# Kernel optimization log

Hardware: AMD Instinct MI355X
Metric: run time of the kernel (lower is better)

## Reference

```python
import jax, jax.numpy as jnp
import numpy as np

GAMMA = 0.9
SCALE_BASE = 512.0


def _xpos(x, downscale=False):
    """XPOS rotary embedding (torchscale variant) applied to x: (B, L, D)."""
    B, L, D = x.shape
    half = D // 2
    # per-channel magnitude base: ((2i) + 0.4*D) / (1.4*D), i over even channels
    scale_vec = (jnp.arange(0, D, 2, dtype=jnp.float32) + 0.4 * D) / (1.4 * D)  # (half,)
    power = jnp.arange(L, dtype=jnp.float32) / SCALE_BASE                        # (L,)
    scale = scale_vec[None, :] ** power[:, None]                                 # (L, half)
    if downscale:
        scale = 1.0 / scale
    # fixed sinusoidal frequencies over `half` dims
    inv_freq = 1.0 / (10000.0 ** (jnp.arange(half, dtype=jnp.float32) / half))   # (half,)
    sinusoid = jnp.arange(L, dtype=jnp.float32)[:, None] * inv_freq[None, :]     # (L, half)
    sin = jnp.repeat(jnp.sin(sinusoid) * scale, 2, axis=-1)                      # (L, D) interleaved dup
    cos = jnp.repeat(jnp.cos(sinusoid) * scale, 2, axis=-1)
    # rotate_every_two: (x0,x1,x2,x3,...) -> (-x1,x0,-x3,x2,...)
    x_even = x[..., 0::2]
    x_odd = x[..., 1::2]
    rot = jnp.stack((-x_odd, x_even), axis=-1).reshape(x.shape)
    return x * cos + rot * sin


def _get_D(seq_len):
    n = jnp.arange(seq_len, dtype=jnp.float32)[:, None]
    m = jnp.arange(seq_len, dtype=jnp.float32)[None, :]
    D = GAMMA ** jnp.abs(n - m)  # non-causal decay, no NaNs since gamma > 0
    return D


def setup_inputs() -> dict:
    key = jax.random.key(0)
    k1, k2, k3, k4 = jax.random.split(key, 4)
    B, L, H, Dh = 8, 2048, 1024, 1024
    X = jax.random.normal(k1, (B, L, H), dtype=jnp.float32)
    W_Q = jax.random.normal(k2, (H, Dh), dtype=jnp.float32) / H
    W_K = jax.random.normal(k3, (H, Dh), dtype=jnp.float32) / H
    W_V = jax.random.normal(k4, (H, Dh), dtype=jnp.float32) / H
    return {"X": X, "W_Q": W_Q, "W_K": W_K, "W_V": W_V}


def reference(X, W_Q, W_K, W_V):
    B, L, H = X.shape
    D = _get_D(L)                       # (L, L)
    Q = _xpos(X @ W_Q)                  # (B, L, Dh)
    K = _xpos(X @ W_K, downscale=True)  # (B, L, Dh)
    V = X @ W_V                         # (B, L, Dv)
    scores = jnp.einsum('bqd,bkd->bqk', Q, K)   # (B, L, L)
    p_attn = jax.nn.softmax(scores, axis=-1)
    p_attn = p_attn * D[None, :, :]              # elementwise decay AFTER softmax
    return jnp.einsum('bqk,bkv->bqv', p_attn, V)
```

## Files before the change

### kernel.cpp

```cpp
#include <hip/hip_runtime.h>
#include <math.h>


#define LDIM 2048
#define HDIM 1024
#define MTOT 16384

typedef unsigned short u16;
typedef __attribute__((ext_vector_type(16))) float f32x16;
typedef __attribute__((ext_vector_type(8))) short s16x8;

#define GLD16(gp, lp) __builtin_amdgcn_global_load_lds( \
    (const __attribute__((address_space(1))) void*)(gp), \
    (__attribute__((address_space(3))) void*)(lp), 16, 0, 0)

__device__ __forceinline__ u16 f2bf(float f) {
    unsigned u = __float_as_uint(f);
    return (u16)((u + 0x7FFFu + ((u >> 16) & 1u)) >> 16);
}

__device__ __forceinline__ void sincos_rev(float ang, float* sn, float* cs) {
    double dr = (double)ang * 0.15915494309189535;
    dr -= __builtin_floor(dr);
    float fr = (float)dr;
    float s_, c_;
    asm("v_sin_f32 %0, %1" : "=v"(s_) : "v"(fr));
    asm("v_cos_f32 %0, %1" : "=v"(c_) : "v"(fr));
    *sn = s_; *cs = c_;
}

#define ROW32(reg, laneHi) (((reg) & 3) + 8 * ((reg) >> 2) + 4 * (laneHi))

__device__ __forceinline__ void gemm128(const u16* __restrict__ A, const u16* __restrict__ B,
                                        int lda, int ldb, int K, int m0, int n0,
                                        char* smem, int tid, f32x16 (*acc)[2])
{
    char* As = smem;
    char* Bs = smem + 128 * 128;
    const int wv = tid >> 6, ln = tid & 63;
    const int wm = wv >> 1, wn = wv & 1;
    const int lane31 = ln & 31, laneHi = ln >> 5;
    const int srow = wv * 8 + (ln >> 3);
    const int scol = ((ln & 7) ^ (ln >> 3)) * 8;

    const u16* ap[4];
    const u16* bp[4];
#pragma unroll
    for (int i = 0; i < 4; ++i) {
        ap[i] = A + (size_t)(m0 + i * 32 + srow) * lda + scol;
        bp[i] = B + (size_t)(n0 + i * 32 + srow) * ldb + scol;
    }

    int abyte[2], bbyte[2];
#pragma unroll
    for (int f = 0; f < 2; ++f) {
        const int row_a = wm * 64 + f * 32 + lane31;
        const int row_b = wn * 64 + f * 32 + lane31;
        const int slot = (laneHi ^ (lane31 & 7)) << 4;
        abyte[f] = row_a * 128 + slot;
        bbyte[f] = row_b * 128 + slot;
    }

    for (int k0 = 0; k0 < K; k0 += 64) {
        __syncthreads();
#pragma unroll
        for (int i = 0; i < 4; ++i) {
            GLD16(ap[i], As + (i * 32 + wv * 8) * 128);
            GLD16(bp[i], Bs + (i * 32 + wv * 8) * 128);
            ap[i] += 64; bp[i] += 64;
        }
        __syncthreads();
#pragma unroll
        for (int ks = 0; ks < 4; ++ks) {
            s16x8 af[2], bf[2];
#pragma unroll
            for (int f = 0; f < 2; ++f) {
                af[f] = *(const s16x8*)(As + (abyte[f] ^ (ks << 5)));
                bf[f] = *(const s16x8*)(Bs + (bbyte[f] ^ (ks << 5)));
            }
#pragma unroll
            for (int i = 0; i < 2; ++i)
#pragma unroll
                for (int j = 0; j < 2; ++j)
                    acc[i][j] = __builtin_amdgcn_mfma_f32_32x32x16_bf16(af[i], bf[j], acc[i][j], 0, 0, 0);
        }
    }
    __syncthreads();
}

__global__ __launch_bounds__(256) void cast_x(const float* __restrict__ X,
                                              u16* __restrict__ Xb, int n4)
{
    int i = blockIdx.x * 256 + threadIdx.x;
    const int stride = gridDim.x * 256;
    for (; i < n4; i += stride) {
        float4 v = ((const float4*)X)[i];
        ushort4 o = make_ushort4(f2bf(v.x), f2bf(v.y), f2bf(v.z), f2bf(v.w));
        ((ushort4*)Xb)[i] = o;
    }
}

__global__ __launch_bounds__(256) void transw(const float* __restrict__ Wq,
                                              const float* __restrict__ Wk,
                                              const float* __restrict__ Wv,
                                              u16* __restrict__ WT)
{
    __shared__ float L[64][65];
    const int z = blockIdx.z;
    const float* Wz = (z == 0) ? Wq : (z == 1) ? Wk : Wv;
    u16* Oz = WT + (size_t)z * HDIM * HDIM;
    const int k0 = blockIdx.y * 64, n0 = blockIdx.x * 64;
    const int t = threadIdx.x;
    const int r_ = t >> 4, c4 = (t & 15) * 4;
#pragma unroll
    for (int it = 0; it < 4; ++it) {
        const int row = it * 16 + r_;
        float4 v = *(const float4*)&Wz[(size_t)(k0 + row) * HDIM + n0 + c4];
        L[row][c4 + 0] = v.x; L[row][c4 + 1] = v.y;
        L[row][c4 + 2] = v.z; L[row][c4 + 3] = v.w;
    }
    __syncthreads();
#pragma unroll
    for (int it = 0; it < 4; ++it) {
        const int orow = it * 16 + r_;
        ushort4 o = make_ushort4(f2bf(L[c4 + 0][orow]), f2bf(L[c4 + 1][orow]),
                                 f2bf(L[c4 + 2][orow]), f2bf(L[c4 + 3][orow]));
        *(ushort4*)&Oz[(size_t)(n0 + orow) * HDIM + k0 + c4] = o;
    }
}

__global__ __launch_bounds__(256) void qkv_gemm(
    const u16* __restrict__ Xb, const u16* __restrict__ WT,
    u16* __restrict__ Qb, u16* __restrict__ Kb, u16* __restrict__ Vt)
{
    __shared__ __align__(16) char smem[128 * 136 * 2];
    const int bid = blockIdx.x;
    const int xcd = bid & 7, t = bid >> 3;
    const int m8 = t & 7;
    const int u_ = t >> 3;
    const int z  = u_ % 3;
    const int v_ = u_ / 3;
    const int n_ = v_ & 7;
    const int mh = v_ >> 3;
    const int m0 = (xcd * 16 + mh * 8 + m8) * 128;
    const int n0 = n_ * 128;
    const int tid = threadIdx.x;

    f32x16 acc[2][2] = {};

    gemm128(Xb, WT + (size_t)z * HDIM * HDIM, HDIM, HDIM, HDIM, m0, n0, smem, tid, acc);

    const int wv = tid >> 6, ln = tid & 63;
    const int wm = wv >> 1, wn = wv & 1;
    const int lane31 = ln & 31, laneHi = ln >> 5;
    u16* T = (u16*)smem;

    if (z < 2) {
        const float pwsgn = (z == 0) ? (1.f / 512.f) : (-1.f / 512.f);
#pragma unroll
        for (int fn = 0; fn < 2; ++fn) {
            const int gc = n0 + wn * 64 + fn * 32 + lane31;
            const int ih = gc >> 1;
            const float invf = exp2f(-13.287712379549449f * (1.f / 512.f) * (float)ih);
            const float l2sv = log2f(((float)(2 * ih) + 409.6f) * (1.f / 1433.6f));
            const float sgn = (gc & 1) ? 1.f : -1.f;
#pragma unroll
            for (int fm = 0; fm < 2; ++fm) {
#pragma unroll
                for (int reg = 0; reg < 16; ++reg) {
                    const int ml = wm * 64 + fm * 32 + ROW32(reg, laneHi);
                    const int lpos = (m0 + ml) & (LDIM - 1);
                    float c = acc[fm][fn][reg];
                    float p = __shfl_xor(c, 1);
                    float sn, cs;
                    sincos_rev((float)lpos * invf, &sn, &cs);
                    float scl = exp2f((float)lpos * pwsgn * l2sv);
                    T[ml * 136 + wn * 64 + fn * 32 + lane31] = f2bf((c * cs + sgn * p * sn) * scl);
                }
            }
        }
    } else {
#pragma unroll
        for (int fn = 0; fn < 2; ++fn)
#pragma unroll
            for (int fm = 0; fm < 2; ++fm)
#pragma unroll
                for (int reg = 0; reg < 16; ++reg)
                    T[(wn * 64 + fn * 32 + lane31) * 136 + wm * 64 + fm * 32 + ROW32(reg, laneHi)] =
                        f2bf(acc[fm][fn][reg]);
    }
    __syncthreads();

    const int row_ = tid >> 4, colb = (tid & 15) * 8;
    if (z < 2) {
        u16* Out = (z == 0) ? Qb : Kb;
#pragma unroll
        for (int g = 0; g < 8; ++g) {
            const int row = g * 16 + row_;
            s16x8 v = *(const s16x8*)&T[row * 136 + colb];
            *(s16x8*)&Out[(size_t)(m0 + row) * HDIM + n0 + colb] = v;
        }
    } else {
        const int b = m0 >> 11, l0 = m0 & (LDIM - 1);
#pragma unroll
        for (int g = 0; g < 8; ++g) {
            const int row = g * 16 + row_;
            s16x8 v = *(const s16x8*)&T[row * 136 + colb];
            *(s16x8*)&Vt[((size_t)b * HDIM + n0 + row) * LDIM + l0 + colb] = v;
        }
    }
}

__global__ __launch_bounds__(256) void qk_gemm(
    const u16* __restrict__ Q, const u16* __restrict__ Km,
    u16* __restrict__ Wm, float* __restrict__ Zp)
{
    __shared__ __align__(16) char smem[128 * 136 * 2];
    __shared__ float Zl[2][128];
    const int bid = blockIdx.x;
    const int b = bid & 7, t = bid >> 3;
    const int mt8 = t & 7;
    const int w_ = t >> 3;
    const int nt = w_ & 15;
    const int mtH = w_ >> 4;
    const int m0 = (mtH * 8 + mt8) * 128;
    const int n0 = nt * 128;
    const int tid = threadIdx.x;

    f32x16 acc[2][2] = {};

    gemm128(Q + (size_t)b * LDIM * HDIM, Km + (size_t)b * LDIM * HDIM,
            HDIM, HDIM, HDIM, m0, n0, smem, tid, acc);

    const int wv = tid >> 6, ln = tid & 63;
    const int wm = wv >> 1, wn = wv & 1;
    const int lane31 = ln & 31, laneHi = ln >> 5;
    u16* T = (u16*)smem;
    const float LOG2E = 1.4426950408889634f;
    const float LOG2G = -0.15200309344504997f;

    float psum[2][16];
#pragma unroll
    for (int fm = 0; fm < 2; ++fm)
#pragma unroll
        for (int reg = 0; reg < 16; ++reg) psum[fm][reg] = 0.f;

#pragma unroll
    for (int fm = 0; fm < 2; ++fm) {
#pragma unroll
        for (int fn = 0; fn < 2; ++fn) {
            const int gk = n0 + wn * 64 + fn * 32 + lane31;
#pragma unroll
            for (int reg = 0; reg < 16; ++reg) {
                const int mloc = wm * 64 + fm * 32 + ROW32(reg, laneHi);
                const int gq = m0 + mloc;
                float t1 = acc[fm][fn][reg] * LOG2E;
                float e = exp2f(t1);
                int dd = gq - gk; dd = dd < 0 ? -dd : dd;
                psum[fm][reg] += e;
                T[mloc * 136 + wn * 64 + fn * 32 + lane31] =
                    f2bf(exp2f(t1 + (float)dd * LOG2G));
            }
        }
    }
#pragma unroll
    for (int fm = 0; fm < 2; ++fm)
#pragma unroll
        for (int reg = 0; reg < 16; ++reg) {
            float s = psum[fm][reg];
            s += __shfl_xor(s, 1); s += __shfl_xor(s, 2);
            s += __shfl_xor(s, 4); s += __shfl_xor(s, 8);
            s += __shfl_xor(s, 16);
            if (lane31 == 0)
                Zl[wn][wm * 64 + fm * 32 + ROW32(reg, laneHi)] = s;
        }
    __syncthreads();

    const int row_ = tid >> 4, colb = (tid & 15) * 8;
#pragma unroll
    for (int g = 0; g < 8; ++g) {
        const int row = g * 16 + row_;
        s16x8 v = *(const s16x8*)&T[row * 136 + colb];
        *(s16x8*)&Wm[((size_t)b * LDIM + m0 + row) * LDIM + n0 + colb] = v;
    }
    if (tid < 128)
        Zp[((size_t)b * 16 + nt) * LDIM + m0 + tid] = Zl[0][tid] + Zl[1][tid];
}

__global__ __launch_bounds__(256) void pv_gemm(
    const u16* __restrict__ Wm, const u16* __restrict__ Vt,
    const float* __restrict__ Zp, float* __restrict__ Out)
{
    __shared__ __align__(16) char smem[128 * 136 * 2];
    __shared__ float Zinv[128];
    const int bid = blockIdx.x;
    const int b = bid & 7, t = bid >> 3;
    const int mt4 = t & 3;
    const int w_ = t >> 2;
    const int nt = w_ & 7;
    const int mtQ = w_ >> 3;
    const int m0 = (mtQ * 4 + mt4) * 128;
    const int n0 = nt * 128;
    const int tid = threadIdx.x;

    if (tid < 128) {
        float zz = 0.f;
#pragma unroll
        for (int nb = 0; nb < 16; ++nb)
            zz += Zp[((size_t)b * 16 + nb) * LDIM + m0 + tid];
        Zinv[tid] = 1.0f / zz;
    }

    f32x16 acc[2][2] = {};

    gemm128(Wm + (size_t)b * LDIM * LDIM, Vt + (size_t)b * HDIM * LDIM,
            LDIM, LDIM, LDIM, m0, n0, smem, tid, acc);

    const int wv = tid >> 6, ln = tid & 63;
    const int wm = wv >> 1, wn = wv & 1;
    const int lane31 = ln & 31, laneHi = ln >> 5;
    float* Ob = Out + (size_t)b * LDIM * HDIM;
#pragma unroll
    for (int fm = 0; fm < 2; ++fm)
#pragma unroll
        for (int fn = 0; fn < 2; ++fn) {
            const int gn = n0 + wn * 64 + fn * 32 + lane31;
#pragma unroll
            for (int reg = 0; reg < 16; ++reg) {
                const int row = wm * 64 + fm * 32 + ROW32(reg, laneHi);
                Ob[(size_t)(m0 + row) * HDIM + gn] = acc[fm][fn][reg] * Zinv[row];
            }
        }
}

extern "C" void kernel_launch(void* const* d_in, const int* in_sizes, int n_in,
                              void* d_out, int out_size, void* d_ws, size_t ws_size,
                              hipStream_t stream)
{
    (void)in_sizes; (void)n_in; (void)out_size; (void)ws_size;
    const float* X  = (const float*)d_in[0];
    const float* Wq = (const float*)d_in[1];
    const float* Wk = (const float*)d_in[2];
    const float* Wv = (const float*)d_in[3];
    char* ws = (char*)d_ws;
    const size_t MB = 1024 * 1024;

    u16* Wmat = (u16*)ws;
    u16* Xb   = (u16*)ws;
    u16* WT   = (u16*)(ws + 32 * MB);
    u16* Qb   = (u16*)(ws + 64 * MB);
    u16* Kb   = (u16*)(ws + 96 * MB);
    u16* Vt   = (u16*)(ws + 128 * MB);
    float* Zp = (float*)(ws + 160 * MB);

    cast_x<<<2048, 256, 0, stream>>>(X, Xb, MTOT * HDIM / 4);
    transw<<<dim3(16, 16, 3), 256, 0, stream>>>(Wq, Wk, Wv, WT);
    qkv_gemm<<<3072, 256, 0, stream>>>(Xb, WT, Qb, Kb, Vt);
    qk_gemm<<<2048, 256, 0, stream>>>(Qb, Kb, Wmat, Zp);
    pv_gemm<<<1024, 256, 0, stream>>>(Wmat, Vt, Zp, (float*)d_out);
}
```

Baseline: 350.5 us.

## Use triple-buffered async LDS ring and 256x128 tiles with 512-thread GEMM blocks

Replaces the single-buffered GEMM mainloop with a three-slot LDS ring. Global-to-LDS loads for stage k+2 are issued while stage k computes, and explicit vmcnt waits with one barrier per step replace the two barriers per step. All three GEMM kernels now use 512-thread blocks with 256x128 output tiles, which halves the number of blocks and improves operand reuse per block. The epilogues, block-index mappings and partial softmax sums are resized to match. The ring needs about 144KB of LDS per block, so only one block fits per CU despite the launch bound hint.

```diff
diff --git a/kernel.cpp b/kernel.cpp
--- a/kernel.cpp
+++ b/kernel.cpp
@@ -31,52 +31,74 @@
 
 #define ROW32(reg, laneHi) (((reg) & 3) + 8 * ((reg) >> 2) + 4 * (laneHi))
 
-__device__ __forceinline__ void gemm128(const u16* __restrict__ A, const u16* __restrict__ B,
-                                        int lda, int ldb, int K, int m0, int n0,
-                                        char* smem, int tid, f32x16 (*acc)[2])
-{
-    char* As = smem;
-    char* Bs = smem + 128 * 128;
+#define SLOT_BYTES 49152
+#define SMEM_BYTES (3 * SLOT_BYTES)
+
+__device__ __forceinline__ void gemm_ring(const u16* __restrict__ A,
+                                          const u16* __restrict__ B,
+                                          int lda, int ldb, int K, int m0, int n0,
+                                          char* smem, int tid, f32x16 (*acc)[2])
+{
     const int wv = tid >> 6, ln = tid & 63;
     const int wm = wv >> 1, wn = wv & 1;
     const int lane31 = ln & 31, laneHi = ln >> 5;
-    const int srow = wv * 8 + (ln >> 3);
     const int scol = ((ln & 7) ^ (ln >> 3)) * 8;
+    const int woff = wv * 8 * 128;
 
     const u16* ap[4];
-    const u16* bp[4];
-#pragma unroll
-    for (int i = 0; i < 4; ++i) {
-        ap[i] = A + (size_t)(m0 + i * 32 + srow) * lda + scol;
-        bp[i] = B + (size_t)(n0 + i * 32 + srow) * ldb + scol;
-    }
+    const u16* bp[2];
+#pragma unroll
+    for (int i = 0; i < 4; ++i)
+        ap[i] = A + (size_t)(m0 + wv * 8 + i * 64 + (ln >> 3)) * lda + scol;
+#pragma unroll
+    for (int j = 0; j < 2; ++j)
+        bp[j] = B + (size_t)(n0 + wv * 8 + j * 64 + (ln >> 3)) * ldb + scol;
 
     int abyte[2], bbyte[2];
+    const int slot_r = (laneHi ^ (lane31 & 7)) << 4;
 #pragma unroll
     for (int f = 0; f < 2; ++f) {
-        const int row_a = wm * 64 + f * 32 + lane31;
-        const int row_b = wn * 64 + f * 32 + lane31;
-        const int slot = (laneHi ^ (lane31 & 7)) << 4;
-        abyte[f] = row_a * 128 + slot;
-        bbyte[f] = row_b * 128 + slot;
-    }
-
-    for (int k0 = 0; k0 < K; k0 += 64) {
-        __syncthreads();
-#pragma unroll
-        for (int i = 0; i < 4; ++i) {
-            GLD16(ap[i], As + (i * 32 + wv * 8) * 128);
-            GLD16(bp[i], Bs + (i * 32 + wv * 8) * 128);
-            ap[i] += 64; bp[i] += 64;
-        }
-        __syncthreads();
+        abyte[f] = (wm * 64 + f * 32 + lane31) * 128 + slot_r;
+        bbyte[f] = 32768 + (wn * 64 + f * 32 + lane31) * 128 + slot_r;
+    }
+
+#define STAGE(sl) do {                                                     \
+        char* base_ = smem + (sl) * SLOT_BYTES;                            \
+        _Pragma("unroll")                                                  \
+        for (int i_ = 0; i_ < 4; ++i_) {                                   \
+            GLD16(ap[i_], base_ + woff + i_ * 8192);                       \
+            ap[i_] += 64;                                                  \
+        }                                                                  \
+        _Pragma("unroll")                                                  \
+        for (int j_ = 0; j_ < 2; ++j_) {                                   \
+            GLD16(bp[j_], base_ + 32768 + woff + j_ * 8192);               \
+            bp[j_] += 64;                                                  \
+        }                                                                  \
+    } while (0)
+
+    const int nk = K >> 6;
+
+    STAGE(0);
+    STAGE(1);
+    asm volatile("s_waitcnt vmcnt(6)" ::: "memory");
+    __builtin_amdgcn_s_barrier();
+    __builtin_amdgcn_sched_barrier(0);
+
+    int sl = 0;
+#pragma unroll 1
+    for (int t = 0; t < nk; ++t) {
+        if (t + 2 < nk) {
+            int s2 = sl + 2; if (s2 >= 3) s2 -= 3;
+            STAGE(s2);
+        }
+        const char* As = smem + sl * SLOT_BYTES;
 #pragma unroll
         for (int ks = 0; ks < 4; ++ks) {
             s16x8 af[2], bf[2];
 #pragma unroll
             for (int f = 0; f < 2; ++f) {
                 af[f] = *(const s16x8*)(As + (abyte[f] ^ (ks << 5)));
-                bf[f] = *(const s16x8*)(Bs + (bbyte[f] ^ (ks << 5)));
+                bf[f] = *(const s16x8*)(As + (bbyte[f] ^ (ks << 5)));
             }
 #pragma unroll
             for (int i = 0; i < 2; ++i)
@@ -84,8 +106,18 @@
                 for (int j = 0; j < 2; ++j)
                     acc[i][j] = __builtin_amdgcn_mfma_f32_32x32x16_bf16(af[i], bf[j], acc[i][j], 0, 0, 0);
         }
+        if (t + 1 < nk) {
+            if (t + 2 < nk)
+                asm volatile("s_waitcnt vmcnt(6)" ::: "memory");
+            else
+                asm volatile("s_waitcnt vmcnt(0)" ::: "memory");
+            __builtin_amdgcn_s_barrier();
+            __builtin_amdgcn_sched_barrier(0);
+        }
+        sl = (sl + 1 == 3) ? 0 : sl + 1;
     }
     __syncthreads();
+#undef STAGE
 }
 
 __global__ __launch_bounds__(256) void cast_x(const float* __restrict__ X,
@@ -129,33 +161,30 @@
     }
 }
 
-__global__ __launch_bounds__(256) void qkv_gemm(
+__global__ __launch_bounds__(512, 2) void qkv_gemm(
     const u16* __restrict__ Xb, const u16* __restrict__ WT,
     u16* __restrict__ Qb, u16* __restrict__ Kb, u16* __restrict__ Vt)
 {
-    __shared__ __align__(16) char smem[128 * 136 * 2];
+    __shared__ __align__(16) char smem[SMEM_BYTES];
     const int bid = blockIdx.x;
     const int xcd = bid & 7, t = bid >> 3;
     const int m8 = t & 7;
-    const int u_ = t >> 3;
-    const int z  = u_ % 3;
-    const int v_ = u_ / 3;
-    const int n_ = v_ & 7;
-    const int mh = v_ >> 3;
-    const int m0 = (xcd * 16 + mh * 8 + m8) * 128;
+    const int n_ = (t >> 3) & 7;
+    const int z  = t >> 6;
+    const int m0 = (xcd * 8 + m8) * 256;
     const int n0 = n_ * 128;
     const int tid = threadIdx.x;
 
     f32x16 acc[2][2] = {};
 
-    gemm128(Xb, WT + (size_t)z * HDIM * HDIM, HDIM, HDIM, HDIM, m0, n0, smem, tid, acc);
+    gemm_ring(Xb, WT + (size_t)z * HDIM * HDIM, HDIM, HDIM, HDIM, m0, n0, smem, tid, acc);
 
     const int wv = tid >> 6, ln = tid & 63;
     const int wm = wv >> 1, wn = wv & 1;
     const int lane31 = ln & 31, laneHi = ln >> 5;
-    u16* T = (u16*)smem;
 
     if (z < 2) {
+        u16* T = (u16*)smem;
         const float pwsgn = (z == 0) ? (1.f / 512.f) : (-1.f / 512.f);
 #pragma unroll
         for (int fn = 0; fn < 2; ++fn) {
@@ -179,58 +208,55 @@
                 }
             }
         }
+        __syncthreads();
+        u16* Out = (z == 0) ? Qb : Kb;
+        const int row_ = tid >> 4, colb = (tid & 15) * 8;
+#pragma unroll
+        for (int g = 0; g < 8; ++g) {
+            const int row = g * 32 + row_;
+            s16x8 v = *(const s16x8*)&T[row * 136 + colb];
+            *(s16x8*)&Out[(size_t)(m0 + row) * HDIM + n0 + colb] = v;
+        }
     } else {
+        u16* T = (u16*)smem;
 #pragma unroll
         for (int fn = 0; fn < 2; ++fn)
 #pragma unroll
             for (int fm = 0; fm < 2; ++fm)
 #pragma unroll
                 for (int reg = 0; reg < 16; ++reg)
-                    T[(wn * 64 + fn * 32 + lane31) * 136 + wm * 64 + fm * 32 + ROW32(reg, laneHi)] =
+                    T[(wn * 64 + fn * 32 + lane31) * 264 + wm * 64 + fm * 32 + ROW32(reg, laneHi)] =
                         f2bf(acc[fm][fn][reg]);
-    }
-    __syncthreads();
-
-    const int row_ = tid >> 4, colb = (tid & 15) * 8;
-    if (z < 2) {
-        u16* Out = (z == 0) ? Qb : Kb;
+        __syncthreads();
+        const int b = m0 >> 11, l0 = m0 & (LDIM - 1);
+        const int row_ = tid >> 5, colb = (tid & 31) * 8;
 #pragma unroll
         for (int g = 0; g < 8; ++g) {
             const int row = g * 16 + row_;
-            s16x8 v = *(const s16x8*)&T[row * 136 + colb];
-            *(s16x8*)&Out[(size_t)(m0 + row) * HDIM + n0 + colb] = v;
-        }
-    } else {
-        const int b = m0 >> 11, l0 = m0 & (LDIM - 1);
-#pragma unroll
-        for (int g = 0; g < 8; ++g) {
-            const int row = g * 16 + row_;
-            s16x8 v = *(const s16x8*)&T[row * 136 + colb];
+            s16x8 v = *(const s16x8*)&T[row * 264 + colb];
             *(s16x8*)&Vt[((size_t)b * HDIM + n0 + row) * LDIM + l0 + colb] = v;
         }
     }
 }
 
-__global__ __launch_bounds__(256) void qk_gemm(
+__global__ __launch_bounds__(512, 2) void qk_gemm(
     const u16* __restrict__ Q, const u16* __restrict__ Km,
     u16* __restrict__ Wm, float* __restrict__ Zp)
 {
-    __shared__ __align__(16) char smem[128 * 136 * 2];
-    __shared__ float Zl[2][128];
+    __shared__ __align__(16) char smem[SMEM_BYTES];
+    __shared__ float Zl[2][256];
     const int bid = blockIdx.x;
     const int b = bid & 7, t = bid >> 3;
-    const int mt8 = t & 7;
-    const int w_ = t >> 3;
-    const int nt = w_ & 15;
-    const int mtH = w_ >> 4;
-    const int m0 = (mtH * 8 + mt8) * 128;
+    const int mt = t & 7;
+    const int nt = t >> 3;
+    const int m0 = mt * 256;
     const int n0 = nt * 128;
     const int tid = threadIdx.x;
 
     f32x16 acc[2][2] = {};
 
-    gemm128(Q + (size_t)b * LDIM * HDIM, Km + (size_t)b * LDIM * HDIM,
-            HDIM, HDIM, HDIM, m0, n0, smem, tid, acc);
+    gemm_ring(Q + (size_t)b * LDIM * HDIM, Km + (size_t)b * LDIM * HDIM,
+              HDIM, HDIM, HDIM, m0, n0, smem, tid, acc);
 
     const int wv = tid >> 6, ln = tid & 63;
     const int wm = wv >> 1, wn = wv & 1;
@@ -279,42 +305,42 @@
     const int row_ = tid >> 4, colb = (tid & 15) * 8;
 #pragma unroll
     for (int g = 0; g < 8; ++g) {
-        const int row = g * 16 + row_;
+        const int row = g * 32 + row_;
         s16x8 v = *(const s16x8*)&T[row * 136 + colb];
         *(s16x8*)&Wm[((size_t)b * LDIM + m0 + row) * LDIM + n0 + colb] = v;
     }
-    if (tid < 128)
+    if (tid < 256)
         Zp[((size_t)b * 16 + nt) * LDIM + m0 + tid] = Zl[0][tid] + Zl[1][tid];
 }
 
-__global__ __launch_bounds__(256) void pv_gemm(
+__global__ __launch_bounds__(512, 2) void pv_gemm(
     const u16* __restrict__ Wm, const u16* __restrict__ Vt,
     const float* __restrict__ Zp, float* __restrict__ Out)
 {
-    __shared__ __align__(16) char smem[128 * 136 * 2];
-    __shared__ float Zinv[128];
+    __shared__ __align__(16) char smem[SMEM_BYTES];
+    __shared__ float Zinv[256];
     const int bid = blockIdx.x;
     const int b = bid & 7, t = bid >> 3;
     const int mt4 = t & 3;
-    const int w_ = t >> 2;
-    const int nt = w_ & 7;
-    const int mtQ = w_ >> 3;
-    const int m0 = (mtQ * 4 + mt4) * 128;
+    const int nt = (t >> 2) & 7;
+    const int mtH = t >> 5;
+    const int m0 = (mtH * 4 + mt4) * 256;
     const int n0 = nt * 128;
     const int tid = threadIdx.x;
 
-    if (tid < 128) {
+    if (tid < 256) {
         float zz = 0.f;
 #pragma unroll
         for (int nb = 0; nb < 16; ++nb)
             zz += Zp[((size_t)b * 16 + nb) * LDIM + m0 + tid];
         Zinv[tid] = 1.0f / zz;
     }
+    __syncthreads();
 
     f32x16 acc[2][2] = {};
 
-    gemm128(Wm + (size_t)b * LDIM * LDIM, Vt + (size_t)b * HDIM * LDIM,
-            LDIM, LDIM, LDIM, m0, n0, smem, tid, acc);
+    gemm_ring(Wm + (size_t)b * LDIM * LDIM, Vt + (size_t)b * HDIM * LDIM,
+              LDIM, LDIM, LDIM, m0, n0, smem, tid, acc);
 
     const int wv = tid >> 6, ln = tid & 63;
     const int wm = wv >> 1, wn = wv & 1;
@@ -355,7 +381,7 @@
 
     cast_x<<<2048, 256, 0, stream>>>(X, Xb, MTOT * HDIM / 4);
     transw<<<dim3(16, 16, 3), 256, 0, stream>>>(Wq, Wk, Wv, WT);
-    qkv_gemm<<<3072, 256, 0, stream>>>(Xb, WT, Qb, Kb, Vt);
-    qk_gemm<<<2048, 256, 0, stream>>>(Qb, Kb, Wmat, Zp);
-    pv_gemm<<<1024, 256, 0, stream>>>(Wmat, Vt, Zp, (float*)d_out);
-}
+    qkv_gemm<<<1536, 512, 0, stream>>>(Xb, WT, Qb, Kb, Vt);
+    qk_gemm<<<1024, 512, 0, stream>>>(Qb, Kb, Wmat, Zp);
+    pv_gemm<<<512, 512, 0, stream>>>(Wmat, Vt, Zp, (float*)d_out);
+}
```

Measured after the change: 398.3 us. 1.14x slower.
